# Kernel optimization log

Hardware: AMD Instinct MI355X
Metric: run time of the kernel (lower is better)

## Reference

```python
import jax, jax.numpy as jnp
import numpy as np

D = 1024
H = 16
HD = D // H
B, K, S = 2, 1024, 4096
EPS = 1e-5


def _ln(x, w, b):
    mu = jnp.mean(x, axis=-1, keepdims=True)
    var = jnp.mean((x - mu) ** 2, axis=-1, keepdims=True)
    return (x - mu) * jax.lax.rsqrt(var + EPS) * w + b


def setup_inputs() -> dict:
    key = jax.random.key(0)
    ks = jax.random.split(key, 16)
    p = lambda k, shape: jax.random.normal(k, shape, dtype=jnp.float32) * 0.02
    return {
        "q": jax.random.normal(ks[0], (B, K, D), dtype=jnp.float32),
        "kv": jax.random.normal(ks[1], (B, S, D), dtype=jnp.float32),
        "attn_bias": jax.random.normal(ks[2], (B, K, S), dtype=jnp.float32),
        "obs_bias": jax.random.normal(ks[3], (B, K, S), dtype=jnp.float32),
        "density": jax.random.uniform(ks[4], (B, K), dtype=jnp.float32),
        "ln_q_w": jnp.ones((D,), jnp.float32), "ln_q_b": jnp.zeros((D,), jnp.float32),
        "ln_kv_w": jnp.ones((D,), jnp.float32), "ln_kv_b": jnp.zeros((D,), jnp.float32),
        "wq": p(ks[5], (D, D)), "bq": jnp.zeros((D,), jnp.float32),
        "wk": p(ks[6], (D, D)), "bk": jnp.zeros((D,), jnp.float32),
        "wv": p(ks[7], (D, D)), "bv": jnp.zeros((D,), jnp.float32),
        "wo": p(ks[8], (D, D)), "bo": jnp.zeros((D,), jnp.float32),
        "dist_raw": jnp.float32(0.0),
        "obs_raw": jnp.float32(0.0),
        "dens_raw": jnp.float32(0.0),
        "ln_f_w": jnp.ones((D,), jnp.float32), "ln_f_b": jnp.zeros((D,), jnp.float32),
        "w1": p(ks[9], (D, 2 * D)), "b1": jnp.zeros((2 * D,), jnp.float32),
        "w2": p(ks[10], (2 * D, D)), "b2": jnp.zeros((D,), jnp.float32),
    }


def reference(q, kv, attn_bias, obs_bias, density,
              ln_q_w, ln_q_b, ln_kv_w, ln_kv_b,
              wq, bq, wk, bk, wv, bv, wo, bo,
              dist_raw, obs_raw, dens_raw,
              ln_f_w, ln_f_b, w1, b1, w2, b2):
    b, k, _ = q.shape
    s = kv.shape[1]
    scale = HD ** (-0.5)

    q_in = _ln(q, ln_q_w, ln_q_b)
    kv_in = _ln(kv, ln_kv_w, ln_kv_b)

    # [B, H, K, HD] / [B, H, S, HD]
    qp = (q_in @ wq + bq).reshape(b, k, H, HD).transpose(0, 2, 1, 3)
    kp = (kv_in @ wk + bk).reshape(b, s, H, HD).transpose(0, 2, 1, 3)
    vp = (kv_in @ wv + bv).reshape(b, s, H, HD).transpose(0, 2, 1, 3)

    scores = jnp.einsum('bhkd,bhsd->bhks', qp, kp) * scale
    scores = scores + jax.nn.softplus(dist_raw) * attn_bias[:, None]
    scores = scores + jax.nn.softplus(obs_raw) * obs_bias[:, None]
    gate = 1.0 + jnp.tanh(dens_raw) * density[:, None, :, None]  # [B,1,K,1]
    scores = scores * gate

    attn = jax.nn.softmax(scores, axis=-1)  # dropout is identity at eval
    out = jnp.einsum('bhks,bhsd->bhkd', attn, vp)
    out = out.transpose(0, 2, 1, 3).reshape(b, k, D) @ wo + bo

    x = q + out
    h = jax.nn.gelu(_ln(x, ln_f_w, ln_f_b) @ w1 + b1, approximate=False)
    x = x + (h @ w2 + b2)
    return x
```

## Files before the change

### kernel.cpp

```cpp
#include <hip/hip_runtime.h>
#include <cstdint>

#define DEV __device__ __forceinline__

typedef __attribute__((ext_vector_type(8))) short bfx8;
typedef __attribute__((ext_vector_type(4))) short bfx4;
typedef __attribute__((ext_vector_type(4))) float fx4;
typedef unsigned short u16;
typedef unsigned int u32;

constexpr int DIM = 1024, NH = 16, HD = 64, BB = 2, KQ = 1024, SEQ = 4096;

DEV u16 f2bf(float f) {
    union { float f; unsigned u; } v{f};
    unsigned r = (v.u + 0x7fffu + ((v.u >> 16) & 1u)) >> 16;
    return (u16)r;
}
DEV float bf2f(u16 s) {
    union { unsigned u; float f; } v{(unsigned)s << 16};
    return v.f;
}
DEV float softplus_f(float x) { return x > 20.f ? x : log1pf(expf(x)); }

#define GLDS(gp, lp)                                                        \
    __builtin_amdgcn_global_load_lds(                                       \
        (const __attribute__((address_space(1))) void*)(gp),                \
        (__attribute__((address_space(3))) void*)(lp), 16, 0, 0)

DEV void wt_body(const float* __restrict__ W, u16* __restrict__ Wt,
                 int Kd, int N, int bx, int by, float* smem) {
    float (*tile)[33] = (float(*)[33])smem;
    const int k0 = by * 32, n0 = bx * 32;
    const int r = threadIdx.x >> 3, c4 = (threadIdx.x & 7) * 4;
    float4 v = *(const float4*)&W[(long)(k0 + r) * N + n0 + c4];
    tile[r][c4 + 0] = v.x; tile[r][c4 + 1] = v.y;
    tile[r][c4 + 2] = v.z; tile[r][c4 + 3] = v.w;
    __syncthreads();
    bfx4 o;
#pragma unroll
    for (int j = 0; j < 4; j++) o[j] = f2bf(tile[c4 + j][r]);
    *(bfx4*)&Wt[(long)(n0 + r) * Kd + k0 + c4] = o;
}

DEV void ln_body(const float* __restrict__ x, const float* __restrict__ w,
                 const float* __restrict__ bsh, u16* __restrict__ out,
                 long row, float* smem) {
    const float4 v = ((const float4*)(x + row * DIM))[threadIdx.x];
    float s1 = v.x + v.y + v.z + v.w;
    float s2 = v.x * v.x + v.y * v.y + v.z * v.z + v.w * v.w;
#pragma unroll
    for (int off = 32; off > 0; off >>= 1) {
        s1 += __shfl_xor(s1, off, 64);
        s2 += __shfl_xor(s2, off, 64);
    }
    if ((threadIdx.x & 63) == 0) {
        smem[threadIdx.x >> 6] = s1;
        smem[4 + (threadIdx.x >> 6)] = s2;
    }
    __syncthreads();
    s1 = smem[0] + smem[1] + smem[2] + smem[3];
    s2 = smem[4] + smem[5] + smem[6] + smem[7];
    float mu = s1 * (1.f / DIM);
    float var = s2 * (1.f / DIM) - mu * mu;
    float rs = rsqrtf(var + 1e-5f);
    int c = threadIdx.x * 4;
    float4 wv = ((const float4*)w)[threadIdx.x];
    float4 bv = ((const float4*)bsh)[threadIdx.x];
    bfx4 o;
    o[0] = f2bf((v.x - mu) * rs * wv.x + bv.x);
    o[1] = f2bf((v.y - mu) * rs * wv.y + bv.y);
    o[2] = f2bf((v.z - mu) * rs * wv.z + bv.z);
    o[3] = f2bf((v.w - mu) * rs * wv.w + bv.w);
    *(bfx4*)&out[row * DIM + c] = o;
}

DEV void cb_body(const float* __restrict__ ab, const float* __restrict__ ob,
                 float c1, float c2, float tgd,
                 const float* __restrict__ density, u16* __restrict__ cb,
                 long i) {
    int row = (int)(i >> 10);
    float g = 1.f + tgd * density[row];
    float4 a = ((const float4*)ab)[i];
    float4 o = ((const float4*)ob)[i];
    bfx4 r;
    r[0] = f2bf((c1 * a.x + c2 * o.x) * g);
    r[1] = f2bf((c1 * a.y + c2 * o.y) * g);
    r[2] = f2bf((c1 * a.z + c2 * o.z) * g);
    r[3] = f2bf((c1 * a.w + c2 * o.w) * g);
    ((bfx4*)cb)[i] = r;
}

__global__ __launch_bounds__(256) void prep_kernel(
    const float* __restrict__ wq, const float* __restrict__ wk,
    const float* __restrict__ wv, const float* __restrict__ wo,
    const float* __restrict__ w1, const float* __restrict__ w2,
    u16* __restrict__ wq_t, u16* __restrict__ wkv_t, u16* __restrict__ wo_t,
    u16* __restrict__ w1_t, u16* __restrict__ w2_t,
    const float* __restrict__ q, const float* __restrict__ lnqw,
    const float* __restrict__ lnqb, u16* __restrict__ q_in,
    const float* __restrict__ kv, const float* __restrict__ lnkw,
    const float* __restrict__ lnkb, u16* __restrict__ kv_in,
    const float* __restrict__ ab, const float* __restrict__ ob,
    const float* __restrict__ dist_raw, const float* __restrict__ obs_raw,
    const float* __restrict__ density, const float* __restrict__ dens_raw,
    u16* __restrict__ cbuf) {
    __shared__ float smem[32 * 33];
    const int id = blockIdx.x;
    if (id < 1024) {
        wt_body(wq, wq_t, DIM, DIM, id & 31, id >> 5, smem);
    } else if (id < 2048) {
        int l = id - 1024;
        wt_body(wk, wkv_t, DIM, DIM, l & 31, l >> 5, smem);
    } else if (id < 3072) {
        int l = id - 2048;
        wt_body(wv, wkv_t + (long)DIM * DIM, DIM, DIM, l & 31, l >> 5, smem);
    } else if (id < 4096) {
        int l = id - 3072;
        wt_body(wo, wo_t, DIM, DIM, l & 31, l >> 5, smem);
    } else if (id < 6144) {
        int l = id - 4096;
        wt_body(w1, w1_t, DIM, 2 * DIM, l & 63, l >> 6, smem);
    } else if (id < 8192) {
        int l = id - 6144;
        wt_body(w2, w2_t, 2 * DIM, DIM, l & 31, l >> 5, smem);
    } else if (id < 10240) {
        ln_body(q, lnqw, lnqb, q_in, id - 8192, smem);
    } else if (id < 18432) {
        ln_body(kv, lnkw, lnkb, kv_in, id - 10240, smem);
    } else {
        const float c1 = softplus_f(dist_raw[0]), c2 = softplus_f(obs_raw[0]);
        const float tgd = tanhf(dens_raw[0]);
        cb_body(ab, ob, c1, c2, tgd, density, cbuf,
                (long)(id - 18432) * 256 + threadIdx.x);
    }
}
constexpr int PREP_BLOCKS = 18432 + (BB * KQ * SEQ / 4) / 256;

__global__ __launch_bounds__(256) void ln_kernel(const float* __restrict__ x,
                                                 const float* __restrict__ w,
                                                 const float* __restrict__ bsh,
                                                 u16* __restrict__ out) {
    __shared__ float smem[8];
    ln_body(x, w, bsh, out, blockIdx.x, smem);
}

template <int MT, int NT, class Epi>
DEV void gemm_body(const u16* __restrict__ A, const u16* __restrict__ Bt,
                   int Kd, Epi epi, int bx, int by, u16* smem) {
    constexpr int MF = MT / 32, NF = NT / 32;
    u16* As = smem;
    u16* Bs = smem + MT * 64;
    const int tid = threadIdx.x;
    const int lane = tid & 63, wave = tid >> 6;
    const int quad = lane >> 4, l16 = lane & 15;
    const int wm = (wave >> 1) * (MT / 2), wn = (wave & 1) * (NT / 2);
    const long row0 = (long)by * MT, col0 = (long)bx * NT;
    const int lr = lane >> 3;
    const int lch = (lane & 7) ^ lr;
    const int sw = (l16 & 7);

    fx4 acc[MF][NF] = {};
    for (int k0 = 0; k0 < Kd; k0 += 64) {
        __syncthreads();
#pragma unroll
        for (int p = 0; p < MF; p++) {
            int ch = wave * MF + p;
            GLDS(&A[(row0 + ch * 8 + lr) * Kd + k0 + lch * 8], &As[ch * 512]);
        }
#pragma unroll
        for (int p = 0; p < NF; p++) {
            int ch = wave * NF + p;
            GLDS(&Bt[(col0 + ch * 8 + lr) * Kd + k0 + lch * 8], &Bs[ch * 512]);
        }
        __syncthreads();
        bfx8 af[2][MF], bfv[2][NF];
#pragma unroll
        for (int kk = 0; kk < 2; kk++) {
#pragma unroll
            for (int m = 0; m < MF; m++)
                af[kk][m] = *(const bfx8*)&As[(wm + m * 16 + l16) * 64 +
                                              (((kk * 4 + quad) ^ sw) * 8)];
#pragma unroll
            for (int n = 0; n < NF; n++)
                bfv[kk][n] = *(const bfx8*)&Bs[(wn + n * 16 + l16) * 64 +
                                               (((kk * 4 + quad) ^ sw) * 8)];
        }
#pragma unroll
        for (int kk = 0; kk < 2; kk++)
#pragma unroll
            for (int m = 0; m < MF; m++)
#pragma unroll
                for (int n = 0; n < NF; n++)
                    acc[m][n] = __builtin_amdgcn_mfma_f32_16x16x32_bf16(
                        af[kk][m], bfv[kk][n], acc[m][n], 0, 0, 0);
    }
#pragma unroll
    for (int m = 0; m < MF; m++)
#pragma unroll
        for (int n = 0; n < NF; n++)
            epi((int)(row0 + wm + m * 16 + quad * 4),
                (int)(col0 + wn + n * 16 + l16), acc[m][n]);
}

template <int MT, int NT, class Epi>
__global__ __launch_bounds__(256) void gemm_bt(const u16* __restrict__ A,
                                               const u16* __restrict__ Bt,
                                               int Kd, Epi epi) {
    __shared__ u16 smem[(MT + NT) * 64];
    gemm_body<MT, NT>(A, Bt, Kd, epi, blockIdx.x, blockIdx.y, smem);
}

struct EpiQp {
    const float* bias; u16* out;
    DEV void operator()(int r0, int c, fx4 v) const {
        float bv = bias[c];
#pragma unroll
        for (int r = 0; r < 4; r++)
            out[(long)(r0 + r) * DIM + c] = f2bf((v[r] + bv) * 0.125f);
    }
};
struct EpiKV {
    const float* bk; const float* bv; u16* kp; u16* vpT;
    DEV void operator()(int r0, int c, fx4 v) const {
        if (c < DIM) {
            float b = bk[c];
#pragma unroll
            for (int r = 0; r < 4; r++)
                kp[(long)(r0 + r) * DIM + c] = f2bf(v[r] + b);
        } else {
            int d = c - DIM;
            float b = bv[d];
            int bi = r0 >> 12, s = r0 & (SEQ - 1);
            bfx4 o;
#pragma unroll
            for (int r = 0; r < 4; r++) o[r] = f2bf(v[r] + b);
            *(bfx4*)&vpT[((long)(bi * DIM + d)) * SEQ + s] = o;
        }
    }
};
struct EpiWo {
    const float* bias; const float* qres; float* x;
    DEV void operator()(int r0, int c, fx4 v) const {
        float bv = bias[c];
#pragma unroll
        for (int r = 0; r < 4; r++) {
            long idx = (long)(r0 + r) * DIM + c;
            x[idx] = qres[idx] + v[r] + bv;
        }
    }
};
struct EpiW1 {
    const float* bias; u16* h;
    DEV void operator()(int r0, int c, fx4 v) const {
        float bv = bias[c];
#pragma unroll
        for (int r = 0; r < 4; r++) {
            float t = v[r] + bv;
            float g = 0.5f * t * (1.f + erff(t * 0.70710678118654752f));
            h[(long)(r0 + r) * (2 * DIM) + c] = f2bf(g);
        }
    }
};
struct EpiW2 {
    const float* bias; const float* x; float* out;
    DEV void operator()(int r0, int c, fx4 v) const {
        float bv = bias[c];
#pragma unroll
        for (int r = 0; r < 4; r++) {
            long idx = (long)(r0 + r) * DIM + c;
            out[idx] = x[idx] + v[r] + bv;
        }
    }
};

__global__ __launch_bounds__(256) void proj_kernel(
    const u16* __restrict__ q_in, const u16* __restrict__ wq_t,
    const float* __restrict__ bq, u16* __restrict__ qp,
    const u16* __restrict__ kv_in, const u16* __restrict__ wkv_t,
    const float* __restrict__ bk, const float* __restrict__ bv,
    u16* __restrict__ kp, u16* __restrict__ vpT) {
    __shared__ u16 smem[(128 + 128) * 64];
    const int id = blockIdx.x;
    if (id < 512) {
        gemm_body<64, 64>(q_in, wq_t, DIM, EpiQp{bq, qp}, id & 15, id >> 4, smem);
    } else {
        int l = id - 512;
        gemm_body<128, 128>(kv_in, wkv_t, DIM, EpiKV{bk, bv, kp, vpT},
                            l & 15, l >> 4, smem);
    }
}

__global__ __launch_bounds__(256, 4) void attn_kernel(
    const u16* __restrict__ qp, const u16* __restrict__ kp,
    const u16* __restrict__ vpT, const u16* __restrict__ cb,
    const float* __restrict__ density, const float* __restrict__ dens_raw,
    float* __restrict__ Opart, float* __restrict__ Lpart) {
    const int b = blockIdx.z, h = blockIdx.y;
    const int q0 = (blockIdx.x >> 1) * 64, sh = blockIdx.x & 1;
    const int sbase = sh * (SEQ / 2);
    const int tid = threadIdx.x, wave = tid >> 6, lane = tid & 63;
    const int quad = lane >> 4, l16 = lane & 15;
    const int lr = lane >> 3, lch = (lane & 7) ^ lr, sw = l16 & 7;
    __shared__ u16 QCb[64 * 64];
    __shared__ u16 Ks[64 * 64], Vs[64 * 64];
    const float tgd = tanhf(dens_raw[0]);

#pragma unroll
    for (int p = 0; p < 2; p++) {
        int ch = wave * 2 + p;
        GLDS(&qp[((long)(b * KQ + q0 + ch * 8 + lr)) * DIM + h * HD + lch * 8],
             &QCb[ch * 512]);
    }
    const float gate = 1.f + tgd * density[b * KQ + q0 + wave * 16 + l16];
    __syncthreads();
    bfx8 bq[2];
#pragma unroll
    for (int kk = 0; kk < 2; kk++)
        bq[kk] = *(const bfx8*)&QCb[(wave * 16 + l16) * 64 +
                                    (((kk * 4 + quad) ^ sw) * 8)];

    const int src0 = l16 + ((quad & 1) << 5);
    const int src1 = src0 + 16;

    float lsum = 0.f;
    fx4 O[4] = {};

    for (int s0 = sbase; s0 < sbase + SEQ / 2; s0 += 64) {
        __syncthreads();
#pragma unroll
        for (int p = 0; p < 2; p++) {
            int ch = wave * 2 + p;
            GLDS(&kp[((long)(b * SEQ + s0 + ch * 8 + lr)) * DIM + h * HD + lch * 8],
                 &Ks[ch * 512]);
            GLDS(&vpT[((long)(b * DIM + h * HD + ch * 8 + lr)) * SEQ + s0 + lch * 8],
                 &Vs[ch * 512]);
            GLDS(&cb[((long)(b * KQ + q0 + ch * 8 + lr)) * SEQ + s0 + lch * 8],
                 &QCb[ch * 512]);
        }
        __syncthreads();
        fx4 sc[4] = {};
#pragma unroll
        for (int sb = 0; sb < 4; sb++)
#pragma unroll
            for (int kk = 0; kk < 2; kk++) {
                bfx8 ak = *(const bfx8*)&Ks[(sb * 16 + l16) * 64 +
                                            (((kk * 4 + quad) ^ sw) * 8)];
                sc[sb] = __builtin_amdgcn_mfma_f32_16x16x32_bf16(ak, bq[kk], sc[sb], 0, 0, 0);
            }
        u32 pr[4][2];
#pragma unroll
        for (int sb = 0; sb < 4; sb++) {
            int cch = (sb * 2 + (quad >> 1)) ^ sw;
            bfx4 cbv = *(const bfx4*)&QCb[(wave * 16 + l16) * 64 + cch * 8 + (quad & 1) * 4];
            float e[4];
#pragma unroll
            for (int r = 0; r < 4; r++) {
                e[r] = __expf(fmaf(sc[sb][r], gate, bf2f(cbv[r])));
                lsum += e[r];
            }
            pr[sb][0] = __builtin_amdgcn_perm(
                __builtin_bit_cast(u32, e[1]), __builtin_bit_cast(u32, e[0]), 0x07060302u);
            pr[sb][1] = __builtin_amdgcn_perm(
                __builtin_bit_cast(u32, e[3]), __builtin_bit_cast(u32, e[2]), 0x07060302u);
        }
#pragma unroll
        for (int kk = 0; kk < 2; kk++) {
            u32 ap32[4];
#pragma unroll
            for (int rp = 0; rp < 2; rp++) {
                u32 tmp = (quad & 2) ? pr[2 * kk + 1][rp] : pr[2 * kk][rp];
                ap32[rp]     = (u32)__shfl((int)tmp, src0, 64);
                ap32[2 + rp] = (u32)__shfl((int)tmp, src1, 64);
            }
            bfx8 ap = __builtin_bit_cast(bfx8, *(const __attribute__((ext_vector_type(4))) u32*)ap32);
#pragma unroll
            for (int d = 0; d < 4; d++) {
                bfx8 bvv = *(const bfx8*)&Vs[(d * 16 + l16) * 64 +
                                             (((kk * 4 + quad) ^ sw) * 8)];
                O[d] = __builtin_amdgcn_mfma_f32_16x16x32_bf16(ap, bvv, O[d], 0, 0, 0);
            }
        }
    }
    lsum += __shfl_xor(lsum, 16, 64);
    lsum += __shfl_xor(lsum, 32, 64);
    if (lane < 16)
        Lpart[((long)sh * BB * NH + b * NH + h) * KQ + q0 + wave * 16 + lane] = lsum;
    float* Op = Opart + (long)sh * BB * KQ * DIM;
#pragma unroll
    for (int d = 0; d < 4; d++)
#pragma unroll
        for (int r = 0; r < 4; r++)
            Op[((long)(b * KQ + q0 + wave * 16 + quad * 4 + r)) * DIM +
               h * HD + d * 16 + l16] = O[d][r];
}

__global__ __launch_bounds__(256) void attn_combine(
    const float* __restrict__ Opart, const float* __restrict__ Lpart,
    u16* __restrict__ aout) {
    long i = (long)blockIdx.x * 256 + threadIdx.x;
    long e = i * 4;
    int row = (int)(e >> 10);
    int h = ((int)e & 1023) >> 6;
    int b = row >> 10, qq = row & 1023;
    long li = ((long)(b * NH + h) << 10) + qq;
    const long half = (long)BB * KQ * DIM;
    float inv = 1.f / (Lpart[li] + Lpart[(long)BB * NH * KQ + li]);
    float4 a = ((const float4*)Opart)[i];
    float4 c = ((const float4*)(Opart + half))[i];
    bfx4 o;
    o[0] = f2bf((a.x + c.x) * inv);
    o[1] = f2bf((a.y + c.y) * inv);
    o[2] = f2bf((a.z + c.z) * inv);
    o[3] = f2bf((a.w + c.w) * inv);
    ((bfx4*)aout)[i] = o;
}

extern "C" void kernel_launch(void* const* d_in, const int* in_sizes, int n_in,
                              void* d_out, int out_size, void* d_ws, size_t ws_size,
                              hipStream_t stream) {
    (void)in_sizes; (void)n_in; (void)out_size; (void)ws_size;
    const float* q        = (const float*)d_in[0];
    const float* kv       = (const float*)d_in[1];
    const float* ab       = (const float*)d_in[2];
    const float* ob       = (const float*)d_in[3];
    const float* dens     = (const float*)d_in[4];
    const float* lnqw     = (const float*)d_in[5];
    const float* lnqb     = (const float*)d_in[6];
    const float* lnkw     = (const float*)d_in[7];
    const float* lnkb     = (const float*)d_in[8];
    const float* wq       = (const float*)d_in[9];
    const float* bq       = (const float*)d_in[10];
    const float* wk       = (const float*)d_in[11];
    const float* bk       = (const float*)d_in[12];
    const float* wv       = (const float*)d_in[13];
    const float* bv       = (const float*)d_in[14];
    const float* wo       = (const float*)d_in[15];
    const float* bo       = (const float*)d_in[16];
    const float* dist_raw = (const float*)d_in[17];
    const float* obs_raw  = (const float*)d_in[18];
    const float* dens_raw = (const float*)d_in[19];
    const float* lnfw     = (const float*)d_in[20];
    const float* lnfb     = (const float*)d_in[21];
    const float* w1       = (const float*)d_in[22];
    const float* b1       = (const float*)d_in[23];
    const float* w2       = (const float*)d_in[24];
    const float* b2       = (const float*)d_in[25];
    float* out = (float*)d_out;

    char* ws = (char*)d_ws;
    const size_t MB = 1u << 20;
    u16* q_in   = (u16*)(ws + 0);
    u16* kv_in  = (u16*)(ws + 4 * MB);
    float* Opart = (float*)(ws + 0);
    float* Lpart = (float*)(ws + 16 * MB);
    u16* wq_t   = (u16*)(ws + 20 * MB);
    u16* wkv_t  = (u16*)(ws + 22 * MB);
    u16* wo_t   = (u16*)(ws + 26 * MB);
    u16* w1_t   = (u16*)(ws + 28 * MB);
    u16* w2_t   = (u16*)(ws + 32 * MB);
    u16* qp     = (u16*)(ws + 36 * MB);
    u16* kp     = (u16*)(ws + 40 * MB);
    u16* vpT    = (u16*)(ws + 56 * MB);
    u16* cbuf   = (u16*)(ws + 72 * MB);
    u16* aout   = (u16*)(ws + 88 * MB);
    float* xb   = (float*)(ws + 92 * MB);
    u16* xn     = (u16*)(ws + 100 * MB);
    u16* hbuf   = (u16*)(ws + 104 * MB);

    prep_kernel<<<PREP_BLOCKS, 256, 0, stream>>>(
        wq, wk, wv, wo, w1, w2, wq_t, wkv_t, wo_t, w1_t, w2_t,
        q, lnqw, lnqb, q_in, kv, lnkw, lnkb, kv_in,
        ab, ob, dist_raw, obs_raw, dens, dens_raw, cbuf);

    proj_kernel<<<1536, 256, 0, stream>>>(
        q_in, wq_t, bq, qp, kv_in, wkv_t, bk, bv, kp, vpT);

    attn_kernel<<<dim3(KQ / 64 * 2, NH, BB), 256, 0, stream>>>(
        qp, kp, vpT, cbuf, dens, dens_raw, Opart, Lpart);
    attn_combine<<<(BB * KQ * DIM / 4) / 256, 256, 0, stream>>>(Opart, Lpart, aout);

    gemm_bt<64, 64><<<dim3(DIM / 64, BB * KQ / 64), 256, 0, stream>>>(
        aout, wo_t, DIM, EpiWo{bo, q, xb});
    ln_kernel<<<BB * KQ, 256, 0, stream>>>(xb, lnfw, lnfb, xn);
    gemm_bt<64, 128><<<dim3(2 * DIM / 128, BB * KQ / 64), 256, 0, stream>>>(
        xn, w1_t, DIM, EpiW1{b1, hbuf});
    gemm_bt<64, 64><<<dim3(DIM / 64, BB * KQ / 64), 256, 0, stream>>>(
        hbuf, w2_t, 2 * DIM, EpiW2{b2, xb, out});
}
```

Baseline: 410.2 us.

## Split attention into four sequence chunks with bf16 partials and direct global Q/bias loads

Each query tile's key range is now split four ways instead of two, doubling the attention grid to improve occupancy and latency hiding, and launch bounds are raised to 6 blocks per CU. The Q fragment and combined bias are read straight from global memory into registers instead of being staged through shared memory, which drops one LDS buffer and a barrier. Partial outputs are stored as bf16 to limit the extra partial-buffer traffic, and the combine kernel sums four partials. The trade-offs are more combine work, uncoalesced per-lane bias reads, and lower precision in the partial accumulators.

```diff
diff --git a/kernel.cpp b/kernel.cpp
--- a/kernel.cpp
+++ b/kernel.cpp
@@ -290,34 +290,27 @@
     }
 }
 
-__global__ __launch_bounds__(256, 4) void attn_kernel(
+__global__ __launch_bounds__(256, 6) void attn_kernel(
     const u16* __restrict__ qp, const u16* __restrict__ kp,
     const u16* __restrict__ vpT, const u16* __restrict__ cb,
     const float* __restrict__ density, const float* __restrict__ dens_raw,
-    float* __restrict__ Opart, float* __restrict__ Lpart) {
+    u16* __restrict__ Opart, float* __restrict__ Lpart) {
     const int b = blockIdx.z, h = blockIdx.y;
-    const int q0 = (blockIdx.x >> 1) * 64, sh = blockIdx.x & 1;
-    const int sbase = sh * (SEQ / 2);
+    const int q0 = (blockIdx.x >> 2) * 64, sh = blockIdx.x & 3;
+    const int sbase = sh * (SEQ / 4);
     const int tid = threadIdx.x, wave = tid >> 6, lane = tid & 63;
     const int quad = lane >> 4, l16 = lane & 15;
     const int lr = lane >> 3, lch = (lane & 7) ^ lr, sw = l16 & 7;
-    __shared__ u16 QCb[64 * 64];
     __shared__ u16 Ks[64 * 64], Vs[64 * 64];
     const float tgd = tanhf(dens_raw[0]);
 
-#pragma unroll
-    for (int p = 0; p < 2; p++) {
-        int ch = wave * 2 + p;
-        GLDS(&qp[((long)(b * KQ + q0 + ch * 8 + lr)) * DIM + h * HD + lch * 8],
-             &QCb[ch * 512]);
-    }
-    const float gate = 1.f + tgd * density[b * KQ + q0 + wave * 16 + l16];
-    __syncthreads();
+    const int myq = q0 + wave * 16 + l16;
+    const float gate = 1.f + tgd * density[b * KQ + myq];
+    const u16* qrp = &qp[((long)(b * KQ) + myq) * DIM + h * HD];
     bfx8 bq[2];
-#pragma unroll
-    for (int kk = 0; kk < 2; kk++)
-        bq[kk] = *(const bfx8*)&QCb[(wave * 16 + l16) * 64 +
-                                    (((kk * 4 + quad) ^ sw) * 8)];
+    bq[0] = *(const bfx8*)&qrp[quad * 8];
+    bq[1] = *(const bfx8*)&qrp[32 + quad * 8];
+    const u16* cbp = &cb[((long)(b * KQ) + myq) * SEQ];
 
     const int src0 = l16 + ((quad & 1) << 5);
     const int src1 = src0 + 16;
@@ -325,7 +318,8 @@
     float lsum = 0.f;
     fx4 O[4] = {};
 
-    for (int s0 = sbase; s0 < sbase + SEQ / 2; s0 += 64) {
+    for (int t = 0; t < SEQ / 4; t += 64) {
+        const int s0 = sbase + t;
         __syncthreads();
 #pragma unroll
         for (int p = 0; p < 2; p++) {
@@ -334,9 +328,11 @@
                  &Ks[ch * 512]);
             GLDS(&vpT[((long)(b * DIM + h * HD + ch * 8 + lr)) * SEQ + s0 + lch * 8],
                  &Vs[ch * 512]);
-            GLDS(&cb[((long)(b * KQ + q0 + ch * 8 + lr)) * SEQ + s0 + lch * 8],
-                 &QCb[ch * 512]);
-        }
+        }
+        bfx4 cbv[4];
+#pragma unroll
+        for (int sb = 0; sb < 4; sb++)
+            cbv[sb] = *(const bfx4*)&cbp[s0 + sb * 16 + quad * 4];
         __syncthreads();
         fx4 sc[4] = {};
 #pragma unroll
@@ -350,12 +346,10 @@
         u32 pr[4][2];
 #pragma unroll
         for (int sb = 0; sb < 4; sb++) {
-            int cch = (sb * 2 + (quad >> 1)) ^ sw;
-            bfx4 cbv = *(const bfx4*)&QCb[(wave * 16 + l16) * 64 + cch * 8 + (quad & 1) * 4];
             float e[4];
 #pragma unroll
             for (int r = 0; r < 4; r++) {
-                e[r] = __expf(fmaf(sc[sb][r], gate, bf2f(cbv[r])));
+                e[r] = __expf(fmaf(sc[sb][r], gate, bf2f(cbv[sb][r])));
                 lsum += e[r];
             }
             pr[sb][0] = __builtin_amdgcn_perm(
@@ -385,17 +379,17 @@
     lsum += __shfl_xor(lsum, 32, 64);
     if (lane < 16)
         Lpart[((long)sh * BB * NH + b * NH + h) * KQ + q0 + wave * 16 + lane] = lsum;
-    float* Op = Opart + (long)sh * BB * KQ * DIM;
+    u16* Op = Opart + (long)sh * BB * KQ * DIM;
 #pragma unroll
     for (int d = 0; d < 4; d++)
 #pragma unroll
         for (int r = 0; r < 4; r++)
             Op[((long)(b * KQ + q0 + wave * 16 + quad * 4 + r)) * DIM +
-               h * HD + d * 16 + l16] = O[d][r];
+               h * HD + d * 16 + l16] = f2bf(O[d][r]);
 }
 
 __global__ __launch_bounds__(256) void attn_combine(
-    const float* __restrict__ Opart, const float* __restrict__ Lpart,
+    const u16* __restrict__ Opart, const float* __restrict__ Lpart,
     u16* __restrict__ aout) {
     long i = (long)blockIdx.x * 256 + threadIdx.x;
     long e = i * 4;
@@ -403,15 +397,20 @@
     int h = ((int)e & 1023) >> 6;
     int b = row >> 10, qq = row & 1023;
     long li = ((long)(b * NH + h) << 10) + qq;
+    const long LS = (long)BB * NH * KQ;
+    float inv = 1.f / (Lpart[li] + Lpart[LS + li] + Lpart[2 * LS + li] +
+                       Lpart[3 * LS + li]);
     const long half = (long)BB * KQ * DIM;
-    float inv = 1.f / (Lpart[li] + Lpart[(long)BB * NH * KQ + li]);
-    float4 a = ((const float4*)Opart)[i];
-    float4 c = ((const float4*)(Opart + half))[i];
+    float acc[4] = {};
+#pragma unroll
+    for (int s = 0; s < 4; s++) {
+        bfx4 v = ((const bfx4*)(Opart + s * half))[i];
+#pragma unroll
+        for (int j = 0; j < 4; j++) acc[j] += bf2f(v[j]);
+    }
     bfx4 o;
-    o[0] = f2bf((a.x + c.x) * inv);
-    o[1] = f2bf((a.y + c.y) * inv);
-    o[2] = f2bf((a.z + c.z) * inv);
-    o[3] = f2bf((a.w + c.w) * inv);
+#pragma unroll
+    for (int j = 0; j < 4; j++) o[j] = f2bf(acc[j] * inv);
     ((bfx4*)aout)[i] = o;
 }
 
@@ -451,7 +450,7 @@
     const size_t MB = 1u << 20;
     u16* q_in   = (u16*)(ws + 0);
     u16* kv_in  = (u16*)(ws + 4 * MB);
-    float* Opart = (float*)(ws + 0);
+    u16* Opart  = (u16*)(ws + 0);
     float* Lpart = (float*)(ws + 16 * MB);
     u16* wq_t   = (u16*)(ws + 20 * MB);
     u16* wkv_t  = (u16*)(ws + 22 * MB);
@@ -475,7 +474,7 @@
     proj_kernel<<<1536, 256, 0, stream>>>(
         q_in, wq_t, bq, qp, kv_in, wkv_t, bk, bv, kp, vpT);
 
-    attn_kernel<<<dim3(KQ / 64 * 2, NH, BB), 256, 0, stream>>>(
+    attn_kernel<<<dim3(KQ / 64 * 4, NH, BB), 256, 0, stream>>>(
         qp, kp, vpT, cbuf, dens, dens_raw, Opart, Lpart);
     attn_combine<<<(BB * KQ * DIM / 4) / 256, 256, 0, stream>>>(Opart, Lpart, aout);
 
```

After: 424.9 us. 3.6% more time.
